# Optimization experiments

Measured on AMD Instinct MI355X. Metric: run time of the kernel, lower is better.

## Reference

```python
import jax, jax.numpy as jnp
import numpy as np

LAMBDA_ORTHO = 0.01
MARGIN = 1.0
T = 8
EPS = 1e-8


def setup_inputs() -> dict:
    key = jax.random.key(0)
    ks = jax.random.split(key, 6)
    B, D, K, N = 4096, 768, 64, 1024
    v = jax.random.normal(ks[0], (B, D), dtype=jnp.float32)
    vhat = jax.random.normal(ks[1], (B, D), dtype=jnp.float32)
    g = jax.random.uniform(ks[2], (B, K), dtype=jnp.float32)
    F = jax.random.normal(ks[3], (K, D), dtype=jnp.float32)
    negatives = jax.random.normal(ks[4], (N, D), dtype=jnp.float32)
    mask = jax.random.randint(ks[5], (B,), 0, 2, dtype=jnp.int32)
    return {"v": v, "vhat": vhat, "g": g, "F": F, "negatives": negatives, "mask": mask}


def _l2(u, w):
    # sqrt(clamp(||u-w||^2, 0) + 1e-8), reducing over last dim
    d2 = jnp.clip(jnp.sum((u - w) ** 2, axis=-1), 0.0)
    return jnp.sqrt(d2 + EPS)


def reference(v, vhat, g, F, negatives, mask):
    maskf = mask.astype(v.dtype)
    msum = jnp.clip(maskf.sum(), 1.0)

    true_d = _l2(vhat, v)  # [B]

    # ---- contrastive loss: vectorized over all N negatives (expansion form of L2) ----
    d2 = (jnp.sum(vhat ** 2, axis=1)[:, None]
          + jnp.sum(negatives ** 2, axis=1)[None, :]
          - 2.0 * vhat @ negatives.T)                      # [B, N]
    neg_d = jnp.sqrt(jnp.clip(d2, 0.0) + EPS)              # [B, N]
    Ju = jnp.mean(jnp.clip(1.0 + true_d[:, None] - neg_d, 0.0), axis=1)  # [B]
    Ju = (Ju * maskf).sum() / msum

    # ---- focal triplet loss: top-t SMALLEST g per row ----
    neg_vals, idx = jax.lax.top_k(-g, T)                   # smallest t, ascending in g
    g_tz = -neg_vals                                       # [B, T]
    F_t = F[idx]                                           # [B, T, D] gather
    g_t = g_tz / (g_tz.sum(axis=1, keepdims=True) + 1e-10)
    m_t = MARGIN * (1.0 - g_t) ** 2                        # [B, T]
    d_neg = _l2(vhat[:, None, :], F_t)                     # [B, T]
    Jt = jnp.mean(jnp.clip(m_t + true_d[:, None] - d_neg, 0.0), axis=1)  # [B]
    Jt = (Jt * maskf).sum() / msum

    # ---- orthogonality: ||F F^T - I||_F^2 ----
    gram = F @ F.T                                          # [K, K]
    ortho = LAMBDA_ORTHO * jnp.sum((gram - jnp.eye(gram.shape[0], dtype=gram.dtype)) ** 2)

    return Ju + Jt + ortho
```

## Files before the change

### kernel.cpp

```cpp
#include <hip/hip_runtime.h>
#include <math.h>

#define KD 768
#define T_SEL 8

typedef float f32x4v __attribute__((ext_vector_type(4)));
typedef __bf16 bf16x8 __attribute__((ext_vector_type(8)));

__device__ __forceinline__ float wave_sum(float x) {
#pragma unroll
  for (int o = 32; o > 0; o >>= 1) x += __shfl_xor(x, o, 64);
  return x;
}

__device__ __forceinline__ unsigned short f2bf(float x) {
  unsigned int u = __float_as_uint(x);
  unsigned int r = (u + 0x7fffu + ((u >> 16) & 1u)) >> 16;
  return (unsigned short)r;
}

__device__ __forceinline__ ushort4 cvt4(float4 a) {
  ushort4 us;
  us.x = f2bf(a.x); us.y = f2bf(a.y); us.z = f2bf(a.z); us.w = f2bf(a.w);
  return us;
}

__device__ __forceinline__ void async_copy16(void* lds, const void* g) {
  __builtin_amdgcn_global_load_lds(
      (const __attribute__((address_space(1))) unsigned int*)g,
      (__attribute__((address_space(3))) unsigned int*)lds, 16, 0, 0);
}

__global__ __launch_bounds__(256) void k_prep(
    const float* __restrict__ v, const float* __restrict__ vhat,
    const float* __restrict__ negs, const float* __restrict__ F,
    unsigned short* __restrict__ A_bf, unsigned short* __restrict__ B_bf,
    float* __restrict__ nv2, float* __restrict__ true_d,
    float* __restrict__ colBn) {
  const int w = threadIdx.x >> 6, l = threadIdx.x & 63;
  const int row = blockIdx.x * 4 + w;
  if (row < 4096) {
    const float4* vr = (const float4*)(vhat + (size_t)row * KD);
    const float4* vv = (const float4*)(v + (size_t)row * KD);
    ushort4* outb = (ushort4*)(A_bf + (size_t)row * KD);
    float s2 = 0.f, td2 = 0.f;
#pragma unroll
    for (int i = 0; i < 3; ++i) {
      float4 a = vr[i * 64 + l];
      float4 b = vv[i * 64 + l];
      s2 += a.x * a.x + a.y * a.y + a.z * a.z + a.w * a.w;
      float dx = a.x - b.x, dy = a.y - b.y, dz = a.z - b.z, dw = a.w - b.w;
      td2 += dx * dx + dy * dy + dz * dz + dw * dw;
      outb[i * 64 + l] = cvt4(a);
    }
    s2 = wave_sum(s2);
    td2 = wave_sum(td2);
    if (l == 0) {
      nv2[row] = s2;
      true_d[row] = sqrtf(fmaxf(td2, 0.f) + 1e-8f);
    }
  } else if (row < 5120) {
    const int r = row - 4096;
    const float4* nr = (const float4*)(negs + (size_t)r * KD);
    ushort4* outb = (ushort4*)(B_bf + (size_t)r * KD);
    float s2 = 0.f;
#pragma unroll
    for (int i = 0; i < 3; ++i) {
      float4 a = nr[i * 64 + l];
      s2 += a.x * a.x + a.y * a.y + a.z * a.z + a.w * a.w;
      outb[i * 64 + l] = cvt4(a);
    }
    s2 = wave_sum(s2);
    if (l == 0) colBn[r] = s2;
  } else if (row < 5184) {
    const int r = row - 5120;
    const float4* fr4 = (const float4*)(F + (size_t)r * KD);
    ushort4* ob1 = (ushort4*)(B_bf + (size_t)(1024 + r) * KD);
    ushort4* ob2 = (ushort4*)(A_bf + (size_t)(4096 + r) * KD);
    float s2 = 0.f;
#pragma unroll
    for (int i = 0; i < 3; ++i) {
      float4 a = fr4[i * 64 + l];
      s2 += a.x * a.x + a.y * a.y + a.z * a.z + a.w * a.w;
      ushort4 us = cvt4(a);
      ob1[i * 64 + l] = us;
      ob2[i * 64 + l] = us;
    }
    s2 = wave_sum(s2);
    if (l == 0) colBn[1024 + r] = s2;
  } else {
    const int r = row - 5184;
    ushort4* outb = (ushort4*)(A_bf + (size_t)(4160 + r) * KD);
    ushort4 z; z.x = 0; z.y = 0; z.z = 0; z.w = 0;
#pragma unroll
    for (int i = 0; i < 3; ++i) outb[i * 64 + l] = z;
  }
}

__global__ __launch_bounds__(256) void k_gemm(
    const unsigned short* __restrict__ Abf, const unsigned short* __restrict__ Bbf,
    const float* __restrict__ nv2, const float* __restrict__ colBn,
    const float* __restrict__ true_d, const int* __restrict__ mask,
    float* __restrict__ S, float* __restrict__ gemm_part, float* __restrict__ or_sum) {
  __shared__ char smem[49152];

  const int tid = threadIdx.x;
  const int w = tid >> 6;
  const int l = tid & 63;
  const int bid = blockIdx.x;
  int tm, tn;
  if (bid < 512) { tm = bid & 31; tn = bid >> 5; }
  else if (bid < 544) { tm = bid - 512; tn = 16; }
  else { tm = 32; tn = 16; }

  const int row0 = tm * 128;
  const int col0 = tn * 64;
  const int wr = w >> 1, wc = w & 1;
  const int lr = l >> 3;
  const int sl = l & 7;

  f32x4v accf[4][2] = {};

#define STAGE(p, kt)                                                                   \
  {                                                                                    \
    char* sA_ = smem + (p)*24576;                                                      \
    char* sB_ = sA_ + 16384;                                                           \
    const int k0_ = (kt)*64;                                                           \
    _Pragma("unroll") for (int i = 0; i < 6; ++i) {                                    \
      const int c = w + i * 4;                                                         \
      if (c < 16) {                                                                    \
        const int rr = c * 8 + lr;                                                     \
        const int ss = sl ^ (rr & 7);                                                  \
        async_copy16(sA_ + c * 1024, Abf + ((size_t)(row0 + rr) * KD + k0_ + ss * 8)); \
      } else {                                                                         \
        const int cc = c - 16;                                                         \
        const int rr = cc * 8 + lr;                                                    \
        const int ss = sl ^ (rr & 7);                                                  \
        async_copy16(sB_ + cc * 1024, Bbf + ((size_t)(col0 + rr) * KD + k0_ + ss * 8));\
      }                                                                                \
    }                                                                                  \
  }

  const int fr = l & 15, fq = l >> 4;
  STAGE(0, 0);
  __syncthreads();
  int cur = 0;
  for (int kt = 0; kt < 12; ++kt) {
    if (kt + 1 < 12) STAGE(cur ^ 1, kt + 1);
    char* sA = smem + cur * 24576;
    char* sB = sA + 16384;
#pragma unroll
    for (int kk = 0; kk < 2; ++kk) {
      bf16x8 af[4], bfr[2];
#pragma unroll
      for (int m = 0; m < 4; ++m) {
        const int rr = wr * 64 + m * 16 + fr;
        const int slot = (fq + kk * 4) ^ (rr & 7);
        af[m] = *(const bf16x8*)(sA + rr * 128 + slot * 16);
      }
#pragma unroll
      for (int n = 0; n < 2; ++n) {
        const int rr = wc * 32 + n * 16 + fr;
        const int slot = (fq + kk * 4) ^ (rr & 7);
        bfr[n] = *(const bf16x8*)(sB + rr * 128 + slot * 16);
      }
#pragma unroll
      for (int m = 0; m < 4; ++m)
#pragma unroll
        for (int n = 0; n < 2; ++n)
          accf[m][n] = __builtin_amdgcn_mfma_f32_16x16x32_bf16(af[m], bfr[n], accf[m][n], 0, 0, 0);
    }
    __syncthreads();
    cur ^= 1;
  }
#undef STAGE

  float local = 0.f;
  if (tn < 16) {
#pragma unroll
    for (int m = 0; m < 4; ++m) {
#pragma unroll
      for (int j = 0; j < 4; ++j) {
        const int grow = row0 + wr * 64 + m * 16 + fq * 4 + j;
        const float nv = nv2[grow];
        const float td = true_d[grow];
        const float mf = (float)mask[grow];
#pragma unroll
        for (int n = 0; n < 2; ++n) {
          const int gcol = col0 + wc * 32 + n * 16 + fr;
          const float s = accf[m][n][j];
          const float d2 = nv + colBn[gcol] - 2.f * s;
          const float dn = sqrtf(fmaxf(d2, 0.f) + 1e-8f);
          local += mf * fmaxf(1.f + td - dn, 0.f);
        }
      }
    }
  } else if (tm < 32) {
#pragma unroll
    for (int m = 0; m < 4; ++m) {
#pragma unroll
      for (int j = 0; j < 4; ++j) {
        const int grow = row0 + wr * 64 + m * 16 + fq * 4 + j;
#pragma unroll
        for (int n = 0; n < 2; ++n) {
          const int gcol = col0 + wc * 32 + n * 16 + fr;
          S[(size_t)grow * 64 + (gcol - 1024)] = accf[m][n][j];
        }
      }
    }
  } else {
#pragma unroll
    for (int m = 0; m < 4; ++m) {
#pragma unroll
      for (int j = 0; j < 4; ++j) {
        const int grow = row0 + wr * 64 + m * 16 + fq * 4 + j;
        if (grow < 4160) {
          const int i2 = grow - 4096;
#pragma unroll
          for (int n = 0; n < 2; ++n) {
            const int j2 = wc * 32 + n * 16 + fr;
            const float d = accf[m][n][j] - ((i2 == j2) ? 1.f : 0.f);
            local += d * d;
          }
        }
      }
    }
  }

  local = wave_sum(local);
  __syncthreads();
  float* red = (float*)smem;
  if (l == 0) red[w] = local;
  __syncthreads();
  if (tid == 0) {
    const float t = red[0] + red[1] + red[2] + red[3];
    if (bid == 544) or_sum[0] = t;
    else gemm_part[bid] = t;
  }
}

__global__ __launch_bounds__(256) void k_jt(
    const float* __restrict__ g, const float* __restrict__ S,
    const float* __restrict__ nv2, const float* __restrict__ true_d,
    const float* __restrict__ colBn, const int* __restrict__ mask,
    float* __restrict__ jt_part, float* __restrict__ ms_part) {
  const int w = threadIdx.x >> 6, l = threadIdx.x & 63;
  const int row = blockIdx.x * 4 + w;
  const float gl = g[(size_t)row * 64 + l];
  int rank = 0;
#pragma unroll
  for (int d = 1; d < 64; ++d) {
    const float o = __shfl_xor(gl, d, 64);
    const int j = l ^ d;
    rank += (o < gl || (o == gl && j < l)) ? 1 : 0;
  }
  const bool sel = rank < T_SEL;
  const float gsum = wave_sum(sel ? gl : 0.f) + 1e-10f;
  const float s = S[(size_t)row * 64 + l];
  const float d2 = nv2[row] + colBn[1024 + l] - 2.f * s;
  const float dneg = sqrtf(fmaxf(d2, 0.f) + 1e-8f);
  const float gt = gl / gsum;
  const float mt = (1.f - gt) * (1.f - gt);
  const float td = true_d[row];
  const float term = sel ? fmaxf(mt + td - dneg, 0.f) : 0.f;
  const float jt = wave_sum(term);
  const float mf = (float)mask[row];

  __shared__ float red[2][4];
  if (l == 0) {
    red[0][w] = jt * mf;
    red[1][w] = mf;
  }
  __syncthreads();
  if (threadIdx.x == 0) {
    jt_part[blockIdx.x] = red[0][0] + red[0][1] + red[0][2] + red[0][3];
    ms_part[blockIdx.x] = red[1][0] + red[1][1] + red[1][2] + red[1][3];
  }
}

__global__ __launch_bounds__(256) void k_final(
    const float* __restrict__ jt_part, const float* __restrict__ ms_part,
    const float* __restrict__ gemm_part, const float* __restrict__ or_sum,
    float* __restrict__ out) {
  const int tid = threadIdx.x;
  float sj = 0.f, sm = 0.f, su = 0.f;
  for (int i = tid; i < 1024; i += 256) {
    sj += jt_part[i];
    sm += ms_part[i];
  }
  for (int i = tid; i < 544; i += 256) su += gemm_part[i];
  sj = wave_sum(sj);
  sm = wave_sum(sm);
  su = wave_sum(su);
  __shared__ float r[3][4];
  const int w = tid >> 6, l = tid & 63;
  if (l == 0) { r[0][w] = sj; r[1][w] = sm; r[2][w] = su; }
  __syncthreads();
  if (tid == 0) {
    const float jt = r[0][0] + r[0][1] + r[0][2] + r[0][3];
    float ms = r[1][0] + r[1][1] + r[1][2] + r[1][3];
    const float ju = r[2][0] + r[2][1] + r[2][2] + r[2][3];
    ms = fmaxf(ms, 1.f);
    out[0] = ju / (1024.f * ms) + jt / (8.f * ms) + 0.01f * or_sum[0];
  }
}

extern "C" void kernel_launch(void* const* d_in, const int* in_sizes, int n_in,
                              void* d_out, int out_size, void* d_ws, size_t ws_size,
                              hipStream_t stream) {
  const float* v = (const float*)d_in[0];
  const float* vhat = (const float*)d_in[1];
  const float* g = (const float*)d_in[2];
  const float* F = (const float*)d_in[3];
  const float* negs = (const float*)d_in[4];
  const int* mask = (const int*)d_in[5];
  float* out = (float*)d_out;

  char* ws = (char*)d_ws;
  float* true_d = (float*)(ws + 0);
  float* nv2 = (float*)(ws + 16384);
  float* colBn = (float*)(ws + 32768);
  float* jt_part = (float*)(ws + 37120);
  float* ms_part = (float*)(ws + 41216);
  float* gemm_part = (float*)(ws + 45312);
  float* or_sum = (float*)(ws + 47616);
  float* S = (float*)(ws + 49152);
  unsigned short* A_bf = (unsigned short*)(ws + 1097728);
  unsigned short* B_bf = (unsigned short*)(ws + 7585792);

  hipLaunchKernelGGL(k_prep, dim3(1312), dim3(256), 0, stream, v, vhat, negs, F,
                     A_bf, B_bf, nv2, true_d, colBn);
  hipLaunchKernelGGL(k_gemm, dim3(545), dim3(256), 0, stream, A_bf, B_bf,
                     nv2, colBn, true_d, mask, S, gemm_part, or_sum);
  hipLaunchKernelGGL(k_jt, dim3(1024), dim3(256), 0, stream, g, S, nv2, true_d,
                     colBn, mask, jt_part, ms_part);
  hipLaunchKernelGGL(k_final, dim3(1), dim3(256), 0, stream, jt_part, ms_part,
                     gemm_part, or_sum, out);
}
```

Before: 102.5 us.

## Remap GEMM tiles per XCD and fold final reduction into k_jt

```diff
diff --git a/kernel.cpp b/kernel.cpp
--- a/kernel.cpp
+++ b/kernel.cpp
@@ -107,10 +107,11 @@
   const int tid = threadIdx.x;
   const int w = tid >> 6;
   const int l = tid & 63;
-  const int bid = blockIdx.x;
+  const int b0 = blockIdx.x;
+  const int ii = b0 >> 3, xcd = b0 & 7;
+  const int t = ((xcd == 0) ? 0 : (69 + (xcd - 1) * 68)) + ii;
   int tm, tn;
-  if (bid < 512) { tm = bid & 31; tn = bid >> 5; }
-  else if (bid < 544) { tm = bid - 512; tn = 16; }
+  if (t < 544) { tm = t / 17; tn = t % 17; }
   else { tm = 32; tn = 16; }
 
   const int row0 = tm * 128;
@@ -233,9 +234,9 @@
   if (l == 0) red[w] = local;
   __syncthreads();
   if (tid == 0) {
-    const float t = red[0] + red[1] + red[2] + red[3];
-    if (bid == 544) or_sum[0] = t;
-    else gemm_part[bid] = t;
+    const float v4 = red[0] + red[1] + red[2] + red[3];
+    if (t == 544) or_sum[0] = v4;
+    else gemm_part[t] = v4;
   }
 }
 
@@ -243,7 +244,9 @@
     const float* __restrict__ g, const float* __restrict__ S,
     const float* __restrict__ nv2, const float* __restrict__ true_d,
     const float* __restrict__ colBn, const int* __restrict__ mask,
-    float* __restrict__ jt_part, float* __restrict__ ms_part) {
+    float* __restrict__ acc, unsigned int* __restrict__ cnt,
+    const float* __restrict__ gemm_part, const float* __restrict__ or_sum,
+    float* __restrict__ out) {
   const int w = threadIdx.x >> 6, l = threadIdx.x & 63;
   const int row = blockIdx.x * 4 + w;
   const float gl = g[(size_t)row * 64 + l];
@@ -267,41 +270,35 @@
   const float mf = (float)mask[row];
 
   __shared__ float red[2][4];
+  __shared__ int last;
   if (l == 0) {
     red[0][w] = jt * mf;
     red[1][w] = mf;
   }
   __syncthreads();
   if (threadIdx.x == 0) {
-    jt_part[blockIdx.x] = red[0][0] + red[0][1] + red[0][2] + red[0][3];
-    ms_part[blockIdx.x] = red[1][0] + red[1][1] + red[1][2] + red[1][3];
-  }
-}
-
-__global__ __launch_bounds__(256) void k_final(
-    const float* __restrict__ jt_part, const float* __restrict__ ms_part,
-    const float* __restrict__ gemm_part, const float* __restrict__ or_sum,
-    float* __restrict__ out) {
-  const int tid = threadIdx.x;
-  float sj = 0.f, sm = 0.f, su = 0.f;
-  for (int i = tid; i < 1024; i += 256) {
-    sj += jt_part[i];
-    sm += ms_part[i];
-  }
-  for (int i = tid; i < 544; i += 256) su += gemm_part[i];
-  sj = wave_sum(sj);
-  sm = wave_sum(sm);
-  su = wave_sum(su);
-  __shared__ float r[3][4];
-  const int w = tid >> 6, l = tid & 63;
-  if (l == 0) { r[0][w] = sj; r[1][w] = sm; r[2][w] = su; }
-  __syncthreads();
-  if (tid == 0) {
-    const float jt = r[0][0] + r[0][1] + r[0][2] + r[0][3];
-    float ms = r[1][0] + r[1][1] + r[1][2] + r[1][3];
-    const float ju = r[2][0] + r[2][1] + r[2][2] + r[2][3];
-    ms = fmaxf(ms, 1.f);
-    out[0] = ju / (1024.f * ms) + jt / (8.f * ms) + 0.01f * or_sum[0];
+    atomicAdd(&acc[0], red[0][0] + red[0][1] + red[0][2] + red[0][3]);
+    atomicAdd(&acc[1], red[1][0] + red[1][1] + red[1][2] + red[1][3]);
+    __threadfence();
+    const unsigned int old = atomicAdd(cnt, 1u);
+    last = (old == (unsigned int)(gridDim.x - 1)) ? 1 : 0;
+  }
+  __syncthreads();
+  if (last) {
+    __threadfence();
+    const int tid = threadIdx.x;
+    float su = 0.f;
+    for (int i = tid; i < 544; i += 256) su += gemm_part[i];
+    su = wave_sum(su);
+    __shared__ float r2[4];
+    if (l == 0) r2[w] = su;
+    __syncthreads();
+    if (tid == 0) {
+      const float ju = r2[0] + r2[1] + r2[2] + r2[3];
+      const float jts = acc[0];
+      const float ms = fmaxf(acc[1], 1.f);
+      out[0] = ju / (1024.f * ms) + jts / (8.f * ms) + 0.01f * or_sum[0];
+    }
   }
 }
 
@@ -320,20 +317,19 @@
   float* true_d = (float*)(ws + 0);
   float* nv2 = (float*)(ws + 16384);
   float* colBn = (float*)(ws + 32768);
-  float* jt_part = (float*)(ws + 37120);
-  float* ms_part = (float*)(ws + 41216);
+  float* acc = (float*)(ws + 37120);
+  unsigned int* cnt = (unsigned int*)(ws + 37128);
   float* gemm_part = (float*)(ws + 45312);
   float* or_sum = (float*)(ws + 47616);
   float* S = (float*)(ws + 49152);
   unsigned short* A_bf = (unsigned short*)(ws + 1097728);
   unsigned short* B_bf = (unsigned short*)(ws + 7585792);
 
+  hipMemsetAsync(acc, 0, 16, stream);
   hipLaunchKernelGGL(k_prep, dim3(1312), dim3(256), 0, stream, v, vhat, negs, F,
                      A_bf, B_bf, nv2, true_d, colBn);
   hipLaunchKernelGGL(k_gemm, dim3(545), dim3(256), 0, stream, A_bf, B_bf,
                      nv2, colBn, true_d, mask, S, gemm_part, or_sum);
   hipLaunchKernelGGL(k_jt, dim3(1024), dim3(256), 0, stream, g, S, nv2, true_d,
-                     colBn, mask, jt_part, ms_part);
-  hipLaunchKernelGGL(k_final, dim3(1), dim3(256), 0, stream, jt_part, ms_part,
-                     gemm_part, or_sum, out);
-}
+                     colBn, mask, acc, cnt, gemm_part, or_sum, out);
+}
```

Result: slower. 143.1 us (+39.5%).
